# Kernel tuning notes

Hardware: AMD Instinct MI355X
Metric: run time of the kernel (lower is better)

Reference implementation:

```python
import jax, jax.numpy as jnp
import numpy as np

BSZ, T, H, P, N = 2, 2048, 16, 64, 64

def setup_inputs() -> dict:
    key = jax.random.key(0)
    k1, k2, k3, k4, k5 = jax.random.split(key, 5)
    X = jax.random.normal(k1, (BSZ, T, H, P), dtype=jnp.float32)
    delta = jax.random.uniform(k2, (BSZ, T, H), dtype=jnp.float32)
    Bmat = jax.random.normal(k3, (BSZ, T, N), dtype=jnp.float32)
    Cmat = jax.random.normal(k4, (BSZ, T, N), dtype=jnp.float32)
    # module init: A_log = log(arange(1, n_heads+1))
    A_log = jnp.log(jnp.arange(1, H + 1, dtype=jnp.float32))
    return {"X": X, "delta": delta, "Bmat": Bmat, "Cmat": Cmat, "A_log": A_log}

def reference(X, delta, Bmat, Cmat, A_log):
    # X: [B,T,H,P], delta: [B,T,H], Bmat/Cmat: [B,T,N], A_log: [H]
    Bsz, Tlen, Hh, Pp = X.shape
    Nn = Bmat.shape[-1]
    dA = jnp.exp(delta * -jnp.exp(A_log))  # [B,T,H] per-step scalar decay

    def step(h, inp):
        dA_t, dt_t, X_t, B_t, C_t = inp  # [B,H], [B,H], [B,H,P], [B,N], [B,N]
        # outer-product input: delta * X outer B -> [B,H,P,N]
        dBx = (dt_t[:, :, None, None] * X_t[..., None]) * B_t[:, None, None, :]
        h = dA_t[:, :, None, None] * h + dBx
        y_t = jnp.einsum('bhpn,bn->bhp', h, C_t)
        return h, y_t

    h0 = jnp.zeros((Bsz, Hh, Pp, Nn), dtype=X.dtype)
    xs = (
        jnp.moveaxis(dA, 1, 0),    # [T,B,H]
        jnp.moveaxis(delta, 1, 0), # [T,B,H]
        jnp.moveaxis(X, 1, 0),     # [T,B,H,P]
        jnp.moveaxis(Bmat, 1, 0),  # [T,B,N]
        jnp.moveaxis(Cmat, 1, 0),  # [T,B,N]
    )
    h_last, ys = jax.lax.scan(step, h0, xs)
    y = jnp.moveaxis(ys, 0, 1)  # [B,T,H,P]
    return y, h_last
```

## Files before the change

### kernel.cpp

```cpp
#include <hip/hip_runtime.h>


constexpr int BSZ = 2, T = 2048, H = 16, P = 64, N = 64;
constexpr int L = 64, NC = T / L;
constexpr int LS = 72;

using bf16x8 = __attribute__((ext_vector_type(8))) short;
using f32x4  = __attribute__((ext_vector_type(4))) float;

__device__ inline ushort f2bf(float f) {
    unsigned u = __float_as_uint(f);
    u += 0x7FFFu + ((u >> 16) & 1u);
    return (ushort)(u >> 16);
}
__device__ inline unsigned pack2(float a, float b) {
    return (unsigned)f2bf(a) | ((unsigned)f2bf(b) << 16);
}
__device__ inline float bf2f(ushort h) {
    return __uint_as_float(((unsigned)h) << 16);
}

__global__ __launch_bounds__(256, 3) void p1_intra(
    const float* __restrict__ X, const float* __restrict__ delta,
    const float* __restrict__ Bm, const float* __restrict__ Cm,
    const float* __restrict__ A_log,
    float* __restrict__ Y, float* __restrict__ Hbuf, float* __restrict__ Dchunk)
{
    __shared__ __align__(16) ushort sB [64 * LS];
    __shared__ __align__(16) ushort sC [64 * LS];
    __shared__ __align__(16) ushort sBt[64 * LS];
    __shared__ __align__(16) ushort sXt[64 * LS];
    __shared__ __align__(16) ushort sS [64 * LS];
    __shared__ float sSa[64], sSb[64], sW[64];

    const int tid  = threadIdx.x, lane = tid & 63, w = tid >> 6;
    const int quad = lane >> 4,   l16  = lane & 15;
    const int blk = blockIdx.x;
    const int h   = blk & (H - 1);
    const int c   = (blk >> 4) & (NC - 1);
    const int b   = blk >> 9;
    const int t0  = c * L;
    const int chunkid = (b * H + h) * NC + c;

    {
        const float4* gB4 = (const float4*)(Bm + ((size_t)b * T + t0) * N);
        const float4* gC4 = (const float4*)(Cm + ((size_t)b * T + t0) * N);
        #pragma unroll
        for (int r = 0; r < 4; ++r) {
            int idx = r * 256 + tid, t = idx >> 4, n4 = (idx & 15) << 2;
            float4 vb = gB4[idx], vc = gC4[idx];
            *(uint2*)&sB[t * LS + n4] = make_uint2(pack2(vb.x, vb.y), pack2(vb.z, vb.w));
            *(uint2*)&sC[t * LS + n4] = make_uint2(pack2(vc.x, vc.y), pack2(vc.z, vc.w));
        }
    }
    {
        const float* gB = Bm + ((size_t)b * T + t0) * N;
        #pragma unroll
        for (int i = 0; i < 8; ++i) {
            int tau = (w * 8 + i) * 2;
            float v0 = gB[(size_t)tau * N + lane];
            float v1 = gB[(size_t)(tau + 1) * N + lane];
            *(unsigned*)&sBt[lane * LS + tau] = pack2(v0, v1);
        }
    }
    {
        const float* gX = X + (((size_t)b * T + t0) * H + h) * P;
        #pragma unroll
        for (int i = 0; i < 8; ++i) {
            int tau = w * 16 + 2 * i;
            float v0 = gX[(size_t)tau * (H * P) + lane];
            float v1 = gX[(size_t)(tau + 1) * (H * P) + lane];
            *(unsigned*)&sXt[lane * LS + tau] = pack2(v0, v1);
        }
    }
    if (w == 0) {
        float dl = delta[((size_t)b * T + t0 + lane) * H + h];
        float s = -__expf(A_log[h]) * dl;
        #pragma unroll
        for (int off = 1; off < 64; off <<= 1) {
            float u = __shfl_up(s, off, 64);
            if (lane >= off) s += u;
        }
        float sL  = __shfl(s, 63, 64);
        float lnd = __logf(dl);
        sSa[lane] = s;
        sSb[lane] = lnd - s;
        sW [lane] = __expf(sL + lnd - s);
        if (lane == 63) Dchunk[chunkid] = __expf(sL);
    }
    __syncthreads();

    f32x4 g[4];
    #pragma unroll
    for (int j = 0; j < 4; ++j) g[j] = (f32x4){0.f, 0.f, 0.f, 0.f};
    #pragma unroll
    for (int ks = 0; ks < 2; ++ks) {
        const int ko = ks * 32 + quad * 8;
        bf16x8 af = *(const bf16x8*)&sC[(w * 16 + l16) * LS + ko];
        #pragma unroll
        for (int jt = 0; jt < 4; ++jt) {
            bf16x8 bfr = *(const bf16x8*)&sB[(jt * 16 + l16) * LS + ko];
            g[jt] = __builtin_amdgcn_mfma_f32_16x16x32_bf16(af, bfr, g[jt], 0, 0, 0);
        }
    }
    #pragma unroll
    for (int jt = 0; jt < 4; ++jt) {
        const int tau = jt * 16 + l16;
        const float sb = sSb[tau];
        #pragma unroll
        for (int r = 0; r < 4; ++r) {
            const int t = w * 16 + quad * 4 + r;
            float arg = (tau <= t) ? (sSa[t] + sb) : -80.0f;
            sS[t * LS + tau] = f2bf(__expf(arg) * g[jt][r]);
        }
    }
    __syncthreads();

    f32x4 ya[4], ha[4];
    #pragma unroll
    for (int j = 0; j < 4; ++j) {
        ya[j] = (f32x4){0.f, 0.f, 0.f, 0.f};
        ha[j] = (f32x4){0.f, 0.f, 0.f, 0.f};
    }
    #pragma unroll
    for (int ks = 0; ks < 2; ++ks) {
        const int ko = ks * 32 + quad * 8;
        bf16x8 sa = *(const bf16x8*)&sS [(w * 16 + l16) * LS + ko];
        bf16x8 xa = *(const bf16x8*)&sXt[(w * 16 + l16) * LS + ko];
        bf16x8 xw;
        #pragma unroll
        for (int j = 0; j < 8; ++j)
            xw[j] = (short)f2bf(bf2f((ushort)xa[j]) * sW[ko + j]);
        #pragma unroll
        for (int jp = 0; jp < 4; ++jp) {
            bf16x8 xb = *(const bf16x8*)&sXt[(jp * 16 + l16) * LS + ko];
            ya[jp] = __builtin_amdgcn_mfma_f32_16x16x32_bf16(sa, xb, ya[jp], 0, 0, 0);
        }
        #pragma unroll
        for (int jn = 0; jn < 4; ++jn) {
            bf16x8 bb = *(const bf16x8*)&sBt[(jn * 16 + l16) * LS + ko];
            ha[jn] = __builtin_amdgcn_mfma_f32_16x16x32_bf16(xw, bb, ha[jn], 0, 0, 0);
        }
    }

    float* Yg = Y + (((size_t)b * T + t0) * H + h) * P;
    #pragma unroll
    for (int jp = 0; jp < 4; ++jp)
        #pragma unroll
        for (int r = 0; r < 4; ++r)
            Yg[(size_t)(w * 16 + quad * 4 + r) * (H * P) + jp * 16 + l16] = ya[jp][r];
    float* Hg = Hbuf + (size_t)chunkid * (P * N);
    #pragma unroll
    for (int jn = 0; jn < 4; ++jn)
        #pragma unroll
        for (int r = 0; r < 4; ++r)
            Hg[(w * 16 + quad * 4 + r) * N + jn * 16 + l16] = ha[jn][r];
}

__global__ __launch_bounds__(256, 4) void p2_scan(
    const float* __restrict__ Dchunk, float* __restrict__ Hbuf,
    float* __restrict__ Hlast)
{
    const int bh  = blockIdx.x >> 4;
    const int rem = ((blockIdx.x & 15) << 8) | threadIdx.x;
    float v[NC];
    #pragma unroll
    for (int c = 0; c < NC; ++c)
        v[c] = Hbuf[(((size_t)(bh * NC + c)) << 12) + rem];
    float hs = 0.0f;
    #pragma unroll
    for (int c = 0; c < NC; ++c) {
        const float tmp = v[c];
        v[c] = hs;
        hs = Dchunk[bh * NC + c] * hs + tmp;
    }
    #pragma unroll
    for (int c = 0; c < NC; ++c)
        Hbuf[(((size_t)(bh * NC + c)) << 12) + rem] = v[c];
    Hlast[(size_t)bh * 4096 + rem] = hs;
}

__global__ __launch_bounds__(256, 4) void p3_inter(
    const float* __restrict__ delta, const float* __restrict__ Cm,
    const float* __restrict__ A_log, const float* __restrict__ Hbuf,
    float* __restrict__ Y)
{
    __shared__ __align__(16) ushort sC[64 * LS];
    __shared__ __align__(16) ushort sH[64 * LS];
    __shared__ float sLam[64];

    const int tid  = threadIdx.x, lane = tid & 63, w = tid >> 6;
    const int quad = lane >> 4,   l16  = lane & 15;
    const int blk = blockIdx.x;
    const int h   = blk & (H - 1);
    const int c   = (blk >> 4) & (NC - 1);
    const int b   = blk >> 9;
    const int t0  = c * L;
    const int chunkid = (b * H + h) * NC + c;

    {
        const float4* gC4 = (const float4*)(Cm + ((size_t)b * T + t0) * N);
        const float4* Hg4 = (const float4*)(Hbuf + (size_t)chunkid * (P * N));
        #pragma unroll
        for (int r = 0; r < 4; ++r) {
            int idx = r * 256 + tid, t = idx >> 4, n4 = (idx & 15) << 2;
            float4 vc = gC4[idx];
            float4 vh = Hg4[idx];
            *(uint2*)&sC[t * LS + n4] = make_uint2(pack2(vc.x, vc.y), pack2(vc.z, vc.w));
            *(uint2*)&sH[t * LS + n4] = make_uint2(pack2(vh.x, vh.y), pack2(vh.z, vh.w));
        }
    }
    if (w == 0) {
        float dl = delta[((size_t)b * T + t0 + lane) * H + h];
        float s = -__expf(A_log[h]) * dl;
        #pragma unroll
        for (int off = 1; off < 64; off <<= 1) {
            float u = __shfl_up(s, off, 64);
            if (lane >= off) s += u;
        }
        sLam[lane] = __expf(s);
    }
    __syncthreads();

    f32x4 acc[4];
    #pragma unroll
    for (int j = 0; j < 4; ++j) acc[j] = (f32x4){0.f, 0.f, 0.f, 0.f};
    #pragma unroll
    for (int ks = 0; ks < 2; ++ks) {
        const int ko = ks * 32 + quad * 8;
        bf16x8 ca = *(const bf16x8*)&sC[(w * 16 + l16) * LS + ko];
        #pragma unroll
        for (int jp = 0; jp < 4; ++jp) {
            bf16x8 hb = *(const bf16x8*)&sH[(jp * 16 + l16) * LS + ko];
            acc[jp] = __builtin_amdgcn_mfma_f32_16x16x32_bf16(ca, hb, acc[jp], 0, 0, 0);
        }
    }

    float* Yg = Y + (((size_t)b * T + t0) * H + h) * P;
    #pragma unroll
    for (int jp = 0; jp < 4; ++jp)
        #pragma unroll
        for (int r = 0; r < 4; ++r) {
            const int t = w * 16 + quad * 4 + r;
            const size_t off = (size_t)t * (H * P) + jp * 16 + l16;
            Yg[off] = Yg[off] + sLam[t] * acc[jp][r];
        }
}

extern "C" void kernel_launch(void* const* d_in, const int* in_sizes, int n_in,
                              void* d_out, int out_size, void* d_ws, size_t ws_size,
                              hipStream_t stream) {
    const float* X     = (const float*)d_in[0];
    const float* delta = (const float*)d_in[1];
    const float* Bm    = (const float*)d_in[2];
    const float* Cm    = (const float*)d_in[3];
    const float* A_log = (const float*)d_in[4];

    float* Y     = (float*)d_out;
    float* Hlast = (float*)d_out + (size_t)BSZ * T * H * P;

    float* Hbuf   = (float*)d_ws;
    float* Dchunk = (float*)d_ws + (size_t)BSZ * H * NC * P * N;

    const int nblk = BSZ * NC * H;
    p1_intra<<<nblk, 256, 0, stream>>>(X, delta, Bm, Cm, A_log, Y, Hbuf, Dchunk);
    p2_scan<<<(BSZ * H * P * N) / 256, 256, 0, stream>>>(Dchunk, Hbuf, Hlast);
    p3_inter<<<nblk, 256, 0, stream>>>(delta, Cm, A_log, Hbuf, Y);
}
```

Before: 103.3 us.

## Fuse intra-chunk, chunk scan and inter-chunk phases into one cooperative kernel

Replaces the three-kernel pipeline with a single cooperative launch that uses grid-wide syncs between the intra-chunk, state-scan and inter-chunk phases. Each 512-thread block processes four heads of one chunk, sharing the staged B/C tiles and keeping the intra-chunk Y in registers so Y is written once instead of read-modified-written. This removes two launches and some global traffic. In exchange it adds two grid barriers, lower occupancy, and a fallback path if the cooperative launch fails.

```diff
diff --git a/kernel.cpp b/kernel.cpp
--- a/kernel.cpp
+++ b/kernel.cpp
@@ -1,4 +1,8 @@
 #include <hip/hip_runtime.h>
+#include <hip/hip_bf16.h>
+#include <hip/hip_cooperative_groups.h>
+
+namespace cg = cooperative_groups;
 
 
 constexpr int BSZ = 2, T = 2048, H = 16, P = 64, N = 64;
@@ -18,6 +22,214 @@
 }
 __device__ inline float bf2f(ushort h) {
     return __uint_as_float(((unsigned)h) << 16);
+}
+
+__global__ __launch_bounds__(512, 1) void fused_ssd(
+    const float* __restrict__ X, const float* __restrict__ delta,
+    const float* __restrict__ Bm, const float* __restrict__ Cm,
+    const float* __restrict__ A_log,
+    float* __restrict__ Y, float* __restrict__ Hlast,
+    float* __restrict__ Hbuf, float* __restrict__ Dchunk)
+{
+    __shared__ __align__(16) ushort sB [64 * LS];
+    __shared__ __align__(16) ushort sC [64 * LS];
+    __shared__ __align__(16) ushort sBt[64 * LS];
+    __shared__ __align__(16) ushort sXt[2][64 * LS];
+    __shared__ __align__(16) ushort sS [2][64 * LS];
+    __shared__ float sSa[2][64], sSb[2][64], sW[2][64], sLam[2][2][64];
+
+    const int tid  = threadIdx.x, lane = tid & 63, w = tid >> 6;
+    const int team = w >> 2,      wv   = w & 3;
+    const int quad = lane >> 4,   l16  = lane & 15;
+    const int idx0  = 4 * blockIdx.x;
+    const int hbase = idx0 & (H - 1);
+    const int c     = (idx0 >> 4) & (NC - 1);
+    const int b     = idx0 >> 9;
+    const int t0    = c * L;
+
+    {
+        const float4* gB4 = (const float4*)(Bm + ((size_t)b * T + t0) * N);
+        const float4* gC4 = (const float4*)(Cm + ((size_t)b * T + t0) * N);
+        #pragma unroll
+        for (int r = 0; r < 2; ++r) {
+            int idx = r * 512 + tid, t = idx >> 4, n4 = (idx & 15) << 2;
+            float4 vb = gB4[idx], vc = gC4[idx];
+            *(uint2*)&sB[t * LS + n4] = make_uint2(pack2(vb.x, vb.y), pack2(vb.z, vb.w));
+            *(uint2*)&sC[t * LS + n4] = make_uint2(pack2(vc.x, vc.y), pack2(vc.z, vc.w));
+        }
+        const float* gB = Bm + ((size_t)b * T + t0) * N;
+        #pragma unroll
+        for (int i = 0; i < 4; ++i) {
+            int tau = (w * 4 + i) * 2;
+            *(unsigned*)&sBt[lane * LS + tau] =
+                pack2(gB[(size_t)tau * N + lane], gB[(size_t)(tau + 1) * N + lane]);
+        }
+    }
+
+    f32x4 ya[2][4];
+
+    #pragma unroll
+    for (int s = 0; s < 2; ++s) {
+        const int h = hbase + 2 * team + s;
+        const int chunkid = (b * H + h) * NC + c;
+
+        {
+            const float* gX = X + (((size_t)b * T + t0) * H + h) * P;
+            #pragma unroll
+            for (int i = 0; i < 8; ++i) {
+                int tau = wv * 16 + 2 * i;
+                *(unsigned*)&sXt[team][lane * LS + tau] =
+                    pack2(gX[(size_t)tau * (H * P) + lane],
+                          gX[(size_t)(tau + 1) * (H * P) + lane]);
+            }
+        }
+        if (wv == 0) {
+            float dl = delta[((size_t)b * T + t0 + lane) * H + h];
+            float sv = -__expf(A_log[h]) * dl;
+            #pragma unroll
+            for (int off = 1; off < 64; off <<= 1) {
+                float u = __shfl_up(sv, off, 64);
+                if (lane >= off) sv += u;
+            }
+            float sL  = __shfl(sv, 63, 64);
+            float lnd = __logf(dl);
+            sSa[team][lane] = sv;
+            sSb[team][lane] = lnd - sv;
+            sW [team][lane] = __expf(sL + lnd - sv);
+            sLam[team][s][lane] = __expf(sv);
+            if (lane == 63) Dchunk[chunkid] = __expf(sL);
+        }
+        __syncthreads();
+
+        f32x4 g[4];
+        #pragma unroll
+        for (int j = 0; j < 4; ++j) g[j] = (f32x4){0.f, 0.f, 0.f, 0.f};
+        #pragma unroll
+        for (int ks = 0; ks < 2; ++ks) {
+            const int ko = ks * 32 + quad * 8;
+            bf16x8 af = *(const bf16x8*)&sC[(wv * 16 + l16) * LS + ko];
+            #pragma unroll
+            for (int jt = 0; jt < 4; ++jt) {
+                bf16x8 bfr = *(const bf16x8*)&sB[(jt * 16 + l16) * LS + ko];
+                g[jt] = __builtin_amdgcn_mfma_f32_16x16x32_bf16(af, bfr, g[jt], 0, 0, 0);
+            }
+        }
+        #pragma unroll
+        for (int jt = 0; jt < 4; ++jt) {
+            const int tau = jt * 16 + l16;
+            const float sbv = sSb[team][tau];
+            #pragma unroll
+            for (int r = 0; r < 4; ++r) {
+                const int t = wv * 16 + quad * 4 + r;
+                float arg = (tau <= t) ? (sSa[team][t] + sbv) : -80.0f;
+                sS[team][t * LS + tau] = f2bf(__expf(arg) * g[jt][r]);
+            }
+        }
+        __syncthreads();
+
+        f32x4 ha[4];
+        #pragma unroll
+        for (int j = 0; j < 4; ++j) {
+            ya[s][j] = (f32x4){0.f, 0.f, 0.f, 0.f};
+            ha[j]    = (f32x4){0.f, 0.f, 0.f, 0.f};
+        }
+        #pragma unroll
+        for (int ks = 0; ks < 2; ++ks) {
+            const int ko = ks * 32 + quad * 8;
+            bf16x8 sa = *(const bf16x8*)&sS [team][(wv * 16 + l16) * LS + ko];
+            bf16x8 xa = *(const bf16x8*)&sXt[team][(wv * 16 + l16) * LS + ko];
+            union { bf16x8 v; unsigned u[4]; } xw;
+            #pragma unroll
+            for (int j2 = 0; j2 < 4; ++j2)
+                xw.u[j2] = pack2(bf2f((ushort)xa[2*j2])   * sW[team][ko + 2*j2],
+                                 bf2f((ushort)xa[2*j2+1]) * sW[team][ko + 2*j2+1]);
+            #pragma unroll
+            for (int jp = 0; jp < 4; ++jp) {
+                bf16x8 xb = *(const bf16x8*)&sXt[team][(jp * 16 + l16) * LS + ko];
+                ya[s][jp] = __builtin_amdgcn_mfma_f32_16x16x32_bf16(sa, xb, ya[s][jp], 0, 0, 0);
+            }
+            #pragma unroll
+            for (int jn = 0; jn < 4; ++jn) {
+                bf16x8 bb = *(const bf16x8*)&sBt[(jn * 16 + l16) * LS + ko];
+                ha[jn] = __builtin_amdgcn_mfma_f32_16x16x32_bf16(xw.v, bb, ha[jn], 0, 0, 0);
+            }
+        }
+        float* Hg = Hbuf + (size_t)chunkid * (P * N);
+        #pragma unroll
+        for (int jn = 0; jn < 4; ++jn)
+            #pragma unroll
+            for (int r = 0; r < 4; ++r)
+                Hg[(wv * 16 + quad * 4 + r) * N + jn * 16 + l16] = ha[jn][r];
+        __syncthreads();
+    }
+
+    cg::grid_group grid = cg::this_grid();
+    grid.sync();
+
+    {
+        const unsigned gid = blockIdx.x * 512u + tid;
+        const int bh  = gid >> 12;
+        const int rem = gid & 4095;
+        float v[NC];
+        #pragma unroll
+        for (int cc = 0; cc < NC; ++cc)
+            v[cc] = Hbuf[((size_t)(bh * NC + cc) << 12) + rem];
+        float hs = 0.0f;
+        #pragma unroll
+        for (int cc = 0; cc < NC; ++cc) {
+            const float tmp = v[cc];
+            v[cc] = hs;
+            hs = Dchunk[bh * NC + cc] * hs + tmp;
+        }
+        #pragma unroll
+        for (int cc = 0; cc < NC; ++cc)
+            Hbuf[((size_t)(bh * NC + cc) << 12) + rem] = v[cc];
+        Hlast[gid] = hs;
+    }
+    grid.sync();
+
+    #pragma unroll
+    for (int s = 0; s < 2; ++s) {
+        const int h = hbase + 2 * team + s;
+        const int chunkid = (b * H + h) * NC + c;
+        ushort* dst = s ? sS[team] : sXt[team];
+        const float4* Hg4 = (const float4*)(Hbuf + (size_t)chunkid * (P * N));
+        const int ttid = wv * 64 + lane;
+        #pragma unroll
+        for (int r = 0; r < 4; ++r) {
+            int idx = r * 256 + ttid, p = idx >> 4, n4 = (idx & 15) << 2;
+            float4 vh = Hg4[idx];
+            *(uint2*)&dst[p * LS + n4] = make_uint2(pack2(vh.x, vh.y), pack2(vh.z, vh.w));
+        }
+    }
+    __syncthreads();
+    #pragma unroll
+    for (int s = 0; s < 2; ++s) {
+        const int h = hbase + 2 * team + s;
+        const ushort* sH = s ? sS[team] : sXt[team];
+        f32x4 acc[4];
+        #pragma unroll
+        for (int j = 0; j < 4; ++j) acc[j] = (f32x4){0.f, 0.f, 0.f, 0.f};
+        #pragma unroll
+        for (int ks = 0; ks < 2; ++ks) {
+            const int ko = ks * 32 + quad * 8;
+            bf16x8 ca = *(const bf16x8*)&sC[(wv * 16 + l16) * LS + ko];
+            #pragma unroll
+            for (int jp = 0; jp < 4; ++jp) {
+                bf16x8 hb = *(const bf16x8*)&sH[(jp * 16 + l16) * LS + ko];
+                acc[jp] = __builtin_amdgcn_mfma_f32_16x16x32_bf16(ca, hb, acc[jp], 0, 0, 0);
+            }
+        }
+        float* Yg = Y + (((size_t)b * T + t0) * H + h) * P;
+        #pragma unroll
+        for (int jp = 0; jp < 4; ++jp)
+            #pragma unroll
+            for (int r = 0; r < 4; ++r) {
+                const int t = wv * 16 + quad * 4 + r;
+                Yg[(size_t)t * (H * P) + jp * 16 + l16] =
+                    ya[s][jp][r] + sLam[team][s][t] * acc[jp][r];
+            }
+    }
 }
 
 __global__ __launch_bounds__(256, 3) void p1_intra(
@@ -52,15 +264,12 @@
             *(uint2*)&sB[t * LS + n4] = make_uint2(pack2(vb.x, vb.y), pack2(vb.z, vb.w));
             *(uint2*)&sC[t * LS + n4] = make_uint2(pack2(vc.x, vc.y), pack2(vc.z, vc.w));
         }
-    }
-    {
         const float* gB = Bm + ((size_t)b * T + t0) * N;
         #pragma unroll
         for (int i = 0; i < 8; ++i) {
             int tau = (w * 8 + i) * 2;
-            float v0 = gB[(size_t)tau * N + lane];
-            float v1 = gB[(size_t)(tau + 1) * N + lane];
-            *(unsigned*)&sBt[lane * LS + tau] = pack2(v0, v1);
+            *(unsigned*)&sBt[lane * LS + tau] =
+                pack2(gB[(size_t)tau * N + lane], gB[(size_t)(tau + 1) * N + lane]);
         }
     }
     {
@@ -68,9 +277,9 @@
         #pragma unroll
         for (int i = 0; i < 8; ++i) {
             int tau = w * 16 + 2 * i;
-            float v0 = gX[(size_t)tau * (H * P) + lane];
-            float v1 = gX[(size_t)(tau + 1) * (H * P) + lane];
-            *(unsigned*)&sXt[lane * LS + tau] = pack2(v0, v1);
+            *(unsigned*)&sXt[lane * LS + tau] =
+                pack2(gX[(size_t)tau * (H * P) + lane],
+                      gX[(size_t)(tau + 1) * (H * P) + lane]);
         }
     }
     if (w == 0) {
@@ -106,11 +315,11 @@
     #pragma unroll
     for (int jt = 0; jt < 4; ++jt) {
         const int tau = jt * 16 + l16;
-        const float sb = sSb[tau];
+        const float sbv = sSb[tau];
         #pragma unroll
         for (int r = 0; r < 4; ++r) {
             const int t = w * 16 + quad * 4 + r;
-            float arg = (tau <= t) ? (sSa[t] + sb) : -80.0f;
+            float arg = (tau <= t) ? (sSa[t] + sbv) : -80.0f;
             sS[t * LS + tau] = f2bf(__expf(arg) * g[jt][r]);
         }
     }
@@ -127,10 +336,11 @@
         const int ko = ks * 32 + quad * 8;
         bf16x8 sa = *(const bf16x8*)&sS [(w * 16 + l16) * LS + ko];
         bf16x8 xa = *(const bf16x8*)&sXt[(w * 16 + l16) * LS + ko];
-        bf16x8 xw;
-        #pragma unroll
-        for (int j = 0; j < 8; ++j)
-            xw[j] = (short)f2bf(bf2f((ushort)xa[j]) * sW[ko + j]);
+        union { bf16x8 v; unsigned u[4]; } xw;
+        #pragma unroll
+        for (int j2 = 0; j2 < 4; ++j2)
+            xw.u[j2] = pack2(bf2f((ushort)xa[2*j2])   * sW[ko + 2*j2],
+                             bf2f((ushort)xa[2*j2+1]) * sW[ko + 2*j2+1]);
         #pragma unroll
         for (int jp = 0; jp < 4; ++jp) {
             bf16x8 xb = *(const bf16x8*)&sXt[(jp * 16 + l16) * LS + ko];
@@ -139,7 +349,7 @@
         #pragma unroll
         for (int jn = 0; jn < 4; ++jn) {
             bf16x8 bb = *(const bf16x8*)&sBt[(jn * 16 + l16) * LS + ko];
-            ha[jn] = __builtin_amdgcn_mfma_f32_16x16x32_bf16(xw, bb, ha[jn], 0, 0, 0);
+            ha[jn] = __builtin_amdgcn_mfma_f32_16x16x32_bf16(xw.v, bb, ha[jn], 0, 0, 0);
         }
     }
 
@@ -258,12 +468,20 @@
 
     float* Y     = (float*)d_out;
     float* Hlast = (float*)d_out + (size_t)BSZ * T * H * P;
-
     float* Hbuf   = (float*)d_ws;
     float* Dchunk = (float*)d_ws + (size_t)BSZ * H * NC * P * N;
 
-    const int nblk = BSZ * NC * H;
-    p1_intra<<<nblk, 256, 0, stream>>>(X, delta, Bm, Cm, A_log, Y, Hbuf, Dchunk);
-    p2_scan<<<(BSZ * H * P * N) / 256, 256, 0, stream>>>(Dchunk, Hbuf, Hlast);
-    p3_inter<<<nblk, 256, 0, stream>>>(delta, Cm, A_log, Hbuf, Y);
-}
+    void* args[] = {(void*)&X, (void*)&delta, (void*)&Bm, (void*)&Cm,
+                    (void*)&A_log, (void*)&Y, (void*)&Hlast,
+                    (void*)&Hbuf, (void*)&Dchunk};
+    hipError_t err = hipLaunchCooperativeKernel(
+        (const void*)fused_ssd, dim3(BSZ * NC * H / 4), dim3(512),
+        args, 0, stream);
+    if (err != hipSuccess) {
+        (void)hipGetLastError();
+        const int nblk = BSZ * NC * H;
+        p1_intra<<<nblk, 256, 0, stream>>>(X, delta, Bm, Cm, A_log, Y, Hbuf, Dchunk);
+        p2_scan<<<(BSZ * H * P * N) / 256, 256, 0, stream>>>(Dchunk, Hbuf, Hlast);
+        p3_inter<<<nblk, 256, 0, stream>>>(delta, Cm, A_log, Hbuf, Y);
+    }
+}
```

Measured after the change: 187.3 us. +81.4%, slower.

## Store intermediate chunk states and partial outputs as bf16 in workspace

Applied to the files above, without the earlier changes.

The intra-chunk kernel now writes its partial Y and chunk states as packed bf16 tiles into a workspace, staged through shared memory for contiguous 16-byte stores, instead of fp32 strided writes. The scan kernel processes two bf16 elements per thread. The inter-chunk kernel reads the bf16 partial Y and adds the inter-chunk term, then writes fp32 Y once with coalesced float4 stores, avoiding the read-modify-write of Y. This cuts intermediate memory traffic at the cost of extra bf16 rounding on states and partial outputs, plus more shared memory and extra barriers.

```diff
diff --git a/kernel.cpp b/kernel.cpp
--- a/kernel.cpp
+++ b/kernel.cpp
@@ -4,6 +4,7 @@
 constexpr int BSZ = 2, T = 2048, H = 16, P = 64, N = 64;
 constexpr int L = 64, NC = T / L;
 constexpr int LS = 72;
+constexpr int FS = 68;
 
 using bf16x8 = __attribute__((ext_vector_type(8))) short;
 using f32x4  = __attribute__((ext_vector_type(4))) float;
@@ -24,7 +25,8 @@
     const float* __restrict__ X, const float* __restrict__ delta,
     const float* __restrict__ Bm, const float* __restrict__ Cm,
     const float* __restrict__ A_log,
-    float* __restrict__ Y, float* __restrict__ Hbuf, float* __restrict__ Dchunk)
+    ushort* __restrict__ Ybuf, ushort* __restrict__ Hbuf,
+    float* __restrict__ Dchunk)
 {
     __shared__ __align__(16) ushort sB [64 * LS];
     __shared__ __align__(16) ushort sC [64 * LS];
@@ -52,15 +54,12 @@
             *(uint2*)&sB[t * LS + n4] = make_uint2(pack2(vb.x, vb.y), pack2(vb.z, vb.w));
             *(uint2*)&sC[t * LS + n4] = make_uint2(pack2(vc.x, vc.y), pack2(vc.z, vc.w));
         }
-    }
-    {
         const float* gB = Bm + ((size_t)b * T + t0) * N;
         #pragma unroll
         for (int i = 0; i < 8; ++i) {
             int tau = (w * 8 + i) * 2;
-            float v0 = gB[(size_t)tau * N + lane];
-            float v1 = gB[(size_t)(tau + 1) * N + lane];
-            *(unsigned*)&sBt[lane * LS + tau] = pack2(v0, v1);
+            *(unsigned*)&sBt[lane * LS + tau] =
+                pack2(gB[(size_t)tau * N + lane], gB[(size_t)(tau + 1) * N + lane]);
         }
     }
     {
@@ -68,9 +67,9 @@
         #pragma unroll
         for (int i = 0; i < 8; ++i) {
             int tau = w * 16 + 2 * i;
-            float v0 = gX[(size_t)tau * (H * P) + lane];
-            float v1 = gX[(size_t)(tau + 1) * (H * P) + lane];
-            *(unsigned*)&sXt[lane * LS + tau] = pack2(v0, v1);
+            *(unsigned*)&sXt[lane * LS + tau] =
+                pack2(gX[(size_t)tau * (H * P) + lane],
+                      gX[(size_t)(tau + 1) * (H * P) + lane]);
         }
     }
     if (w == 0) {
@@ -106,11 +105,11 @@
     #pragma unroll
     for (int jt = 0; jt < 4; ++jt) {
         const int tau = jt * 16 + l16;
-        const float sb = sSb[tau];
+        const float sbv = sSb[tau];
         #pragma unroll
         for (int r = 0; r < 4; ++r) {
             const int t = w * 16 + quad * 4 + r;
-            float arg = (tau <= t) ? (sSa[t] + sb) : -80.0f;
+            float arg = (tau <= t) ? (sSa[t] + sbv) : -80.0f;
             sS[t * LS + tau] = f2bf(__expf(arg) * g[jt][r]);
         }
     }
@@ -127,10 +126,11 @@
         const int ko = ks * 32 + quad * 8;
         bf16x8 sa = *(const bf16x8*)&sS [(w * 16 + l16) * LS + ko];
         bf16x8 xa = *(const bf16x8*)&sXt[(w * 16 + l16) * LS + ko];
-        bf16x8 xw;
-        #pragma unroll
-        for (int j = 0; j < 8; ++j)
-            xw[j] = (short)f2bf(bf2f((ushort)xa[j]) * sW[ko + j]);
+        union { bf16x8 v; unsigned u[4]; } xw;
+        #pragma unroll
+        for (int j2 = 0; j2 < 4; ++j2)
+            xw.u[j2] = pack2(bf2f((ushort)xa[2*j2])   * sW[ko + 2*j2],
+                             bf2f((ushort)xa[2*j2+1]) * sW[ko + 2*j2+1]);
         #pragma unroll
         for (int jp = 0; jp < 4; ++jp) {
             bf16x8 xb = *(const bf16x8*)&sXt[(jp * 16 + l16) * LS + ko];
@@ -139,54 +139,69 @@
         #pragma unroll
         for (int jn = 0; jn < 4; ++jn) {
             bf16x8 bb = *(const bf16x8*)&sBt[(jn * 16 + l16) * LS + ko];
-            ha[jn] = __builtin_amdgcn_mfma_f32_16x16x32_bf16(xw, bb, ha[jn], 0, 0, 0);
-        }
-    }
-
-    float* Yg = Y + (((size_t)b * T + t0) * H + h) * P;
+            ha[jn] = __builtin_amdgcn_mfma_f32_16x16x32_bf16(xw.v, bb, ha[jn], 0, 0, 0);
+        }
+    }
+
+    __syncthreads();
     #pragma unroll
     for (int jp = 0; jp < 4; ++jp)
         #pragma unroll
         for (int r = 0; r < 4; ++r)
-            Yg[(size_t)(w * 16 + quad * 4 + r) * (H * P) + jp * 16 + l16] = ya[jp][r];
-    float* Hg = Hbuf + (size_t)chunkid * (P * N);
+            sS[(w * 16 + quad * 4 + r) * LS + jp * 16 + l16] = f2bf(ya[jp][r]);
     #pragma unroll
     for (int jn = 0; jn < 4; ++jn)
         #pragma unroll
         for (int r = 0; r < 4; ++r)
-            Hg[(w * 16 + quad * 4 + r) * N + jn * 16 + l16] = ha[jn][r];
+            sXt[(w * 16 + quad * 4 + r) * LS + jn * 16 + l16] = f2bf(ha[jn][r]);
+    __syncthreads();
+    ushort* Yt = Ybuf + (size_t)chunkid * 4096;
+    ushort* Ht = Hbuf + (size_t)chunkid * 4096;
+    #pragma unroll
+    for (int i = 0; i < 2; ++i) {
+        int j = i * 256 + tid, t = j >> 3, col = (j & 7) * 8;
+        *(uint4*)&Yt[j * 8] = *(const uint4*)&sS [t * LS + col];
+        *(uint4*)&Ht[j * 8] = *(const uint4*)&sXt[t * LS + col];
+    }
 }
 
 __global__ __launch_bounds__(256, 4) void p2_scan(
-    const float* __restrict__ Dchunk, float* __restrict__ Hbuf,
+    const float* __restrict__ Dchunk, ushort* __restrict__ Hbuf,
     float* __restrict__ Hlast)
 {
-    const int bh  = blockIdx.x >> 4;
-    const int rem = ((blockIdx.x & 15) << 8) | threadIdx.x;
-    float v[NC];
-    #pragma unroll
-    for (int c = 0; c < NC; ++c)
-        v[c] = Hbuf[(((size_t)(bh * NC + c)) << 12) + rem];
-    float hs = 0.0f;
-    #pragma unroll
-    for (int c = 0; c < NC; ++c) {
-        const float tmp = v[c];
-        v[c] = hs;
-        hs = Dchunk[bh * NC + c] * hs + tmp;
-    }
-    #pragma unroll
-    for (int c = 0; c < NC; ++c)
-        Hbuf[(((size_t)(bh * NC + c)) << 12) + rem] = v[c];
-    Hlast[(size_t)bh * 4096 + rem] = hs;
-}
-
-__global__ __launch_bounds__(256, 4) void p3_inter(
+    const unsigned gid = blockIdx.x * 256u + threadIdx.x;
+    const int bh  = gid >> 11;
+    const int rem = gid & 2047;
+    unsigned* Hb = (unsigned*)Hbuf;
+    unsigned v[NC];
+    #pragma unroll
+    for (int cc = 0; cc < NC; ++cc)
+        v[cc] = Hb[(size_t)(bh * NC + cc) * 2048 + rem];
+    float hx = 0.f, hy = 0.f;
+    #pragma unroll
+    for (int cc = 0; cc < NC; ++cc) {
+        const float lo = bf2f((ushort)(v[cc] & 0xffffu));
+        const float hi = bf2f((ushort)(v[cc] >> 16));
+        v[cc] = pack2(hx, hy);
+        const float D = Dchunk[bh * NC + cc];
+        hx = D * hx + lo;
+        hy = D * hy + hi;
+    }
+    #pragma unroll
+    for (int cc = 0; cc < NC; ++cc)
+        Hb[(size_t)(bh * NC + cc) * 2048 + rem] = v[cc];
+    ((float2*)Hlast)[gid] = make_float2(hx, hy);
+}
+
+__global__ __launch_bounds__(256, 3) void p3_inter(
     const float* __restrict__ delta, const float* __restrict__ Cm,
-    const float* __restrict__ A_log, const float* __restrict__ Hbuf,
-    float* __restrict__ Y)
+    const float* __restrict__ A_log, const ushort* __restrict__ Hbuf,
+    const ushort* __restrict__ Ybuf, float* __restrict__ Y)
 {
-    __shared__ __align__(16) ushort sC[64 * LS];
-    __shared__ __align__(16) ushort sH[64 * LS];
+    __shared__ __align__(16) ushort sC [64 * LS];
+    __shared__ __align__(16) ushort sH [64 * LS];
+    __shared__ __align__(16) ushort sYi[64 * LS];
+    __shared__ __align__(16) float  sF [64 * FS];
     __shared__ float sLam[64];
 
     const int tid  = threadIdx.x, lane = tid & 63, w = tid >> 6;
@@ -200,14 +215,19 @@
 
     {
         const float4* gC4 = (const float4*)(Cm + ((size_t)b * T + t0) * N);
-        const float4* Hg4 = (const float4*)(Hbuf + (size_t)chunkid * (P * N));
         #pragma unroll
         for (int r = 0; r < 4; ++r) {
             int idx = r * 256 + tid, t = idx >> 4, n4 = (idx & 15) << 2;
             float4 vc = gC4[idx];
-            float4 vh = Hg4[idx];
             *(uint2*)&sC[t * LS + n4] = make_uint2(pack2(vc.x, vc.y), pack2(vc.z, vc.w));
-            *(uint2*)&sH[t * LS + n4] = make_uint2(pack2(vh.x, vh.y), pack2(vh.z, vh.w));
+        }
+        const uint4* Hg4 = (const uint4*)(Hbuf + (size_t)chunkid * 4096);
+        const uint4* Yg4 = (const uint4*)(Ybuf + (size_t)chunkid * 4096);
+        #pragma unroll
+        for (int i = 0; i < 2; ++i) {
+            int j = i * 256 + tid, t = j >> 3, col = (j & 7) * 8;
+            *(uint4*)&sH [t * LS + col] = Hg4[j];
+            *(uint4*)&sYi[t * LS + col] = Yg4[j];
         }
     }
     if (w == 0) {
@@ -236,15 +256,23 @@
         }
     }
 
-    float* Yg = Y + (((size_t)b * T + t0) * H + h) * P;
     #pragma unroll
     for (int jp = 0; jp < 4; ++jp)
         #pragma unroll
         for (int r = 0; r < 4; ++r) {
             const int t = w * 16 + quad * 4 + r;
-            const size_t off = (size_t)t * (H * P) + jp * 16 + l16;
-            Yg[off] = Yg[off] + sLam[t] * acc[jp][r];
-        }
+            const int p = jp * 16 + l16;
+            sF[t * FS + p] = bf2f(sYi[t * LS + p]) + sLam[t] * acc[jp][r];
+        }
+    __syncthreads();
+
+    float* Yg = Y + (((size_t)b * T + t0) * H + h) * P;
+    #pragma unroll
+    for (int i = 0; i < 4; ++i) {
+        int j = i * 256 + tid, t = j >> 4, c4 = j & 15;
+        *(float4*)(Yg + (size_t)t * (H * P) + c4 * 4) =
+            *(const float4*)&sF[t * FS + c4 * 4];
+    }
 }
 
 extern "C" void kernel_launch(void* const* d_in, const int* in_sizes, int n_in,
@@ -259,11 +287,14 @@
     float* Y     = (float*)d_out;
     float* Hlast = (float*)d_out + (size_t)BSZ * T * H * P;
 
-    float* Hbuf   = (float*)d_ws;
-    float* Dchunk = (float*)d_ws + (size_t)BSZ * H * NC * P * N;
+    constexpr size_t TILE = 4096;
+    constexpr size_t NTILE = (size_t)BSZ * H * NC;
+    ushort* Hbuf = (ushort*)d_ws;
+    ushort* Ybuf = (ushort*)d_ws + NTILE * TILE;
+    float* Dchunk = (float*)((char*)d_ws + 2 * NTILE * TILE * sizeof(ushort));
 
     const int nblk = BSZ * NC * H;
-    p1_intra<<<nblk, 256, 0, stream>>>(X, delta, Bm, Cm, A_log, Y, Hbuf, Dchunk);
-    p2_scan<<<(BSZ * H * P * N) / 256, 256, 0, stream>>>(Dchunk, Hbuf, Hlast);
-    p3_inter<<<nblk, 256, 0, stream>>>(delta, Cm, A_log, Hbuf, Y);
-}
+    p1_intra<<<nblk, 256, 0, stream>>>(X, delta, Bm, Cm, A_log, Ybuf, Hbuf, Dchunk);
+    p2_scan<<<(BSZ * H * P * N / 2) / 256, 256, 0, stream>>>(Dchunk, Hbuf, Hlast);
+    p3_inter<<<nblk, 256, 0, stream>>>(delta, Cm, A_log, Hbuf, Ybuf, Y);
+}
```

Result: faster. 100.3 us (-2.8%).
